# Kernel optimization log

Measured on AMD Instinct MI355X. Metric: run time of the kernel, lower is better.

## Reference

```python
import jax, jax.numpy as jnp
import numpy as np


def setup_inputs() -> dict:
    key = jax.random.key(0)
    kq, kk, kv, km, kb = jax.random.split(key, 5)
    B, H, S, D = 4, 16, 2048, 64
    Q = jax.random.normal(kq, (B, H, S, D), dtype=jnp.float32)
    K = jax.random.normal(kk, (B, H, S, D), dtype=jnp.float32)
    V = jax.random.normal(kv, (B, H, S, D), dtype=jnp.float32)
    # key-padding style mask, broadcasts over query dim; 0 -> masked
    mask = jax.random.randint(km, (B, 1, 1, S), 0, 2, dtype=jnp.int32)
    attn_bias = jax.random.normal(kb, (1, H, S, S), dtype=jnp.float32)
    return {"Q": Q, "K": K, "V": V, "mask": mask, "attn_bias": attn_bias}


def reference(Q, K, V, mask, attn_bias):
    d_k = Q.shape[-1]
    scale = 1.0 / jnp.sqrt(jnp.asarray(d_k, Q.dtype))
    # [B,H,Sq,Sk] scores
    scores = jnp.einsum("bhqd,bhkd->bhqk", Q, K) * scale
    scores = scores + attn_bias
    scores = jnp.where(mask == 0, jnp.asarray(-1e9, scores.dtype), scores)
    attn = jax.nn.softmax(scores, axis=-1)
    # dropout is identity in eval/reference mode
    output = jnp.einsum("bhqk,bhkd->bhqd", attn, V)
    return output, attn
```

## Files before the change

kernel.cpp:

```cpp
#include <hip/hip_runtime.h>

#define NB 4
#define NH 16
#define NS 2048
#define ND 64
#define PST 2052

typedef __attribute__((ext_vector_type(8))) short short8;
typedef __attribute__((ext_vector_type(4))) short short4v;
typedef __attribute__((ext_vector_type(4))) float floatx4;
typedef __attribute__((ext_vector_type(2))) float floatx2;

__device__ __forceinline__ unsigned short f2bf(float f) {
  unsigned u = __builtin_bit_cast(unsigned, f);
  u = (u + 0x7FFFu + ((u >> 16) & 1u)) >> 16;
  return (unsigned short)u;
}
__device__ __forceinline__ float bf2f(unsigned short s) {
  unsigned u = ((unsigned)s) << 16;
  return __builtin_bit_cast(float, u);
}

__global__ __launch_bounds__(256) void prep_k_kernel(const float* __restrict__ K,
                                                     unsigned short* __restrict__ kb) {
  size_t i = ((size_t)blockIdx.x * 256 + threadIdx.x) * 4;
  floatx4 v = *(const floatx4*)(K + i);
  unsigned long long o = 0;
  o |= (unsigned long long)f2bf(v[0]);
  o |= (unsigned long long)f2bf(v[1]) << 16;
  o |= (unsigned long long)f2bf(v[2]) << 32;
  o |= (unsigned long long)f2bf(v[3]) << 48;
  *(unsigned long long*)(kb + i) = o;
}

__global__ __launch_bounds__(256) void prep_vt_kernel(const float* __restrict__ V,
                                                      unsigned short* __restrict__ vt) {
  __shared__ float tile[64][65];
  int kc = blockIdx.x & 31;
  int bh = blockIdx.x >> 5;
  int k0 = kc * 64;
  const float* src = V + ((size_t)bh * NS + k0) * ND;
  int t = threadIdx.x;
  int r0 = t >> 4;
  int c = (t & 15) * 4;
  for (int rr = 0; rr < 4; ++rr) {
    int r = rr * 16 + r0;
    floatx4 v = *(const floatx4*)(src + (size_t)r * ND + c);
    tile[r][c + 0] = v[0]; tile[r][c + 1] = v[1];
    tile[r][c + 2] = v[2]; tile[r][c + 3] = v[3];
  }
  __syncthreads();
  unsigned short* dst = vt + (size_t)bh * ND * NS + k0;
  for (int i = 0; i < 16; ++i) {
    int lin = i * 256 + t;
    int d = lin >> 6, k = lin & 63;
    dst[(size_t)d * NS + k] = f2bf(tile[k][d]);
  }
}

__global__ __launch_bounds__(512, 4) void attn_kernel(
    const float* __restrict__ Q,
    const unsigned short* __restrict__ Kb,
    const unsigned short* __restrict__ VT,
    const int* __restrict__ mask,
    const float* __restrict__ bias,
    float* __restrict__ out,
    float* __restrict__ attn) {
  extern __shared__ char smem[];
  unsigned short* P = (unsigned short*)smem;
  float* sums = (float*)(smem + 16 * PST * 2);

  const int bid = blockIdx.x;
  const int b = bid & 3;
  const int qt = (bid >> 2) & 127;
  const int h = bid >> 9;
  const int q0 = qt * 16;

  const int tid = threadIdx.x;
  const int wave = tid >> 6;
  const int lane = tid & 63;
  const int lg = lane >> 4;
  const int lc = lane & 15;
  const int lg4 = lg * 4;
  const int lg8 = lg * 8;

  const size_t bh = (size_t)(b * NH + h);

  short8 aq[2];
  {
    const float* qrow = Q + (bh * NS + (size_t)(q0 + lc)) * ND + lg8;
#pragma unroll
    for (int t = 0; t < 2; ++t) {
      floatx4 f0 = *(const floatx4*)(qrow + t * 32);
      floatx4 f1 = *(const floatx4*)(qrow + t * 32 + 4);
      short8 a;
      a[0] = (short)f2bf(f0[0]); a[1] = (short)f2bf(f0[1]);
      a[2] = (short)f2bf(f0[2]); a[3] = (short)f2bf(f0[3]);
      a[4] = (short)f2bf(f1[0]); a[5] = (short)f2bf(f1[1]);
      a[6] = (short)f2bf(f1[2]); a[7] = (short)f2bf(f1[3]);
      aq[t] = a;
    }
  }

  const unsigned short* kp = Kb + bh * NS * ND + (size_t)lc * ND + lg8;
  const float* bprow = bias + ((size_t)h * NS + (size_t)(q0 + lg4)) * NS + lc;
  const int* mp = mask + b * NS + lc;
  const int kb0 = wave * 256;

  float psum[4] = {0.f, 0.f, 0.f, 0.f};

  short8 rka[4], rkb[4];
  floatx4 rbv[4];
  int rmv[4];
#pragma unroll
  for (int i = 0; i < 3; ++i) {
    const int k0 = kb0 + i * 16;
    rka[i] = *(const short8*)(kp + (size_t)k0 * ND);
    rkb[i] = *(const short8*)(kp + (size_t)k0 * ND + 32);
    rmv[i] = mp[k0];
    floatx4 bv;
#pragma unroll
    for (int r = 0; r < 4; ++r) bv[r] = bprow[(size_t)r * NS + k0];
    rbv[i] = bv;
  }
#pragma unroll
  for (int it = 0; it < 16; ++it) {
    const int s = it & 3;
    if (it < 13) {
      const int ps = (it + 3) & 3;
      const int k1 = kb0 + (it + 3) * 16;
      rka[ps] = *(const short8*)(kp + (size_t)k1 * ND);
      rkb[ps] = *(const short8*)(kp + (size_t)k1 * ND + 32);
      rmv[ps] = mp[k1];
      floatx4 bv;
#pragma unroll
      for (int r = 0; r < 4; ++r) bv[r] = bprow[(size_t)r * NS + k1];
      rbv[ps] = bv;
    }
    const int k0 = kb0 + it * 16;
    floatx4 c = {0.f, 0.f, 0.f, 0.f};
    c = __builtin_amdgcn_mfma_f32_16x16x32_bf16(aq[0], rka[s], c, 0, 0, 0);
    c = __builtin_amdgcn_mfma_f32_16x16x32_bf16(aq[1], rkb[s], c, 0, 0, 0);
    const int mv = rmv[s];
#pragma unroll
    for (int r = 0; r < 4; ++r) {
      float sc = c[r] * 0.125f + rbv[s][r];
      float p = mv ? __expf(sc) : 0.f;
      psum[r] += p;
      P[(lg4 + r) * PST + k0 + lc] = f2bf(p);
    }
  }

#pragma unroll
  for (int r = 0; r < 4; ++r) {
    float v = psum[r];
    v += __shfl_xor(v, 1);
    v += __shfl_xor(v, 2);
    v += __shfl_xor(v, 4);
    v += __shfl_xor(v, 8);
    if (lc == 0) sums[wave * 16 + lg4 + r] = v;
  }
  __syncthreads();

  const int wrow0 = wave * 2;
  float inv0, inv1;
  {
    float t0 = 0.f, t1 = 0.f;
#pragma unroll
    for (int w = 0; w < 8; ++w) {
      t0 += sums[w * 16 + wrow0];
      t1 += sums[w * 16 + wrow0 + 1];
    }
    inv0 = 1.f / t0;
    inv1 = 1.f / t1;
  }

  const size_t abase = (bh * NS + (size_t)q0) * NS;

#define WRITECHUNK(c)                                                        \
  {                                                                          \
    const int row_ = wrow0 + ((c) >> 3);                                     \
    const float inv_ = (((c) >> 3) == 0) ? inv0 : inv1;                      \
    const int col_ = ((c) & 7) * 256 + lane * 4;                             \
    short4v pv_ = *(const short4v*)(P + row_ * PST + col_);                  \
    floatx4 f_;                                                              \
    f_[0] = bf2f((unsigned short)pv_[0]) * inv_;                             \
    f_[1] = bf2f((unsigned short)pv_[1]) * inv_;                             \
    f_[2] = bf2f((unsigned short)pv_[2]) * inv_;                             \
    f_[3] = bf2f((unsigned short)pv_[3]) * inv_;                             \
    __builtin_nontemporal_store(f_, (floatx4*)(attn + abase +                \
                                               (size_t)row_ * NS + col_));   \
  }

  floatx4 o[4];
#pragma unroll
  for (int dt = 0; dt < 4; ++dt) o[dt] = (floatx4){0.f, 0.f, 0.f, 0.f};

  const unsigned short* vp = VT + bh * (size_t)ND * NS + (size_t)lc * NS + lg8;
  short8 vt0[4], vt1[4];
#pragma unroll
  for (int dt = 0; dt < 4; ++dt)
    vt0[dt] = *(const short8*)(vp + (size_t)(dt * 16) * NS + kb0);

#pragma unroll
  for (int ih = 0; ih < 4; ++ih) {
    const int itA = ih * 2, itB = ih * 2 + 1;
    const int k0A = kb0 + itA * 32, k0B = kb0 + itB * 32;
#pragma unroll
    for (int dt = 0; dt < 4; ++dt)
      vt1[dt] = *(const short8*)(vp + (size_t)(dt * 16) * NS + k0B);
    WRITECHUNK(ih * 4 + 0);
    WRITECHUNK(ih * 4 + 1);
    {
      const unsigned short* pr = P + lc * PST + k0A + lg8;
      short4v lo = *(const short4v*)pr;
      short4v hi = *(const short4v*)(pr + 4);
      short8 pa = __builtin_shufflevector(lo, hi, 0, 1, 2, 3, 4, 5, 6, 7);
#pragma unroll
      for (int dt = 0; dt < 4; ++dt)
        o[dt] = __builtin_amdgcn_mfma_f32_16x16x32_bf16(pa, vt0[dt], o[dt], 0, 0, 0);
    }
    if (ih < 3) {
      const int k0N = kb0 + (ih + 1) * 64;
#pragma unroll
      for (int dt = 0; dt < 4; ++dt)
        vt0[dt] = *(const short8*)(vp + (size_t)(dt * 16) * NS + k0N);
    }
    WRITECHUNK(ih * 4 + 2);
    WRITECHUNK(ih * 4 + 3);
    {
      const unsigned short* pr = P + lc * PST + k0B + lg8;
      short4v lo = *(const short4v*)pr;
      short4v hi = *(const short4v*)(pr + 4);
      short8 pa = __builtin_shufflevector(lo, hi, 0, 1, 2, 3, 4, 5, 6, 7);
#pragma unroll
      for (int dt = 0; dt < 4; ++dt)
        o[dt] = __builtin_amdgcn_mfma_f32_16x16x32_bf16(pa, vt1[dt], o[dt], 0, 0, 0);
    }
  }
#undef WRITECHUNK

  __syncthreads();

  float* Ored = (float*)smem;
#pragma unroll
  for (int dt = 0; dt < 4; ++dt)
#pragma unroll
    for (int r = 0; r < 4; ++r)
      Ored[((size_t)wave * 16 + lg4 + r) * 64 + dt * 16 + lc] = o[dt][r];
  __syncthreads();

  {
    const int q = tid >> 5;
    const int c2 = (tid & 31) * 2;
    floatx2 acc = {0.f, 0.f};
#pragma unroll
    for (int w = 0; w < 8; ++w) {
      const float* p = Ored + ((size_t)w * 16 + q) * 64 + c2;
      acc[0] += p[0];
      acc[1] += p[1];
    }
    float tot = 0.f;
#pragma unroll
    for (int w = 0; w < 8; ++w) tot += sums[w * 16 + q];
    const float inv = 1.f / tot;
    floatx2 res;
    res[0] = acc[0] * inv;
    res[1] = acc[1] * inv;
    __builtin_nontemporal_store(res, (floatx2*)(out + (bh * NS + (size_t)(q0 + q)) * ND + c2));
  }
}

extern "C" void kernel_launch(void* const* d_in, const int* in_sizes, int n_in,
                              void* d_out, int out_size, void* d_ws, size_t ws_size,
                              hipStream_t stream) {
  const float* Q = (const float*)d_in[0];
  const float* K = (const float*)d_in[1];
  const float* V = (const float*)d_in[2];
  const int* mask = (const int*)d_in[3];
  const float* bias = (const float*)d_in[4];

  float* out = (float*)d_out;
  float* attn = out + (size_t)NB * NH * NS * ND;

  unsigned short* kb = (unsigned short*)d_ws;
  unsigned short* vt = kb + (size_t)NB * NH * NS * ND;

  const int lds_bytes = 16 * PST * 2 + 8 * 16 * 4;
  (void)hipFuncSetAttribute((const void*)attn_kernel,
                            hipFuncAttributeMaxDynamicSharedMemorySize, lds_bytes);

  prep_k_kernel<<<(NB * NH * NS * ND) / (256 * 4), 256, 0, stream>>>(K, kb);
  prep_vt_kernel<<<NB * NH * (NS / 64), 256, 0, stream>>>(V, vt);
  attn_kernel<<<NB * NH * (NS / 16), 512, lds_bytes, stream>>>(Q, kb, vt, mask, bias, out, attn);
}
```

Baseline: 634.4 us.

## Transpose QK MFMA so bias and mask load as vectors, fold scale into Q

Swaps the MFMA operand order in the QK^T stage so each lane holds four consecutive keys for one query row. Bias and mask can then be read as 16-byte vectors, and the bias is used directly as the MFMA accumulator init. The 1/sqrt(d) scale is folded into Q before the bf16 conversion, and the row-sum reduction is simplified. The loops are manually unrolled into explicit register buffers with compiler memory fences to control load scheduling. Applying the scale before rounding to bf16 changes rounding slightly, and the fences may restrict compiler reordering.

Result: slower. 846.1 us (+33.4%).

```diff
diff --git a/kernel.cpp b/kernel.cpp
--- a/kernel.cpp
+++ b/kernel.cpp
@@ -10,6 +10,8 @@
 typedef __attribute__((ext_vector_type(4))) short short4v;
 typedef __attribute__((ext_vector_type(4))) float floatx4;
 typedef __attribute__((ext_vector_type(2))) float floatx2;
+typedef __attribute__((ext_vector_type(4))) int intx4;
+typedef __attribute__((ext_vector_type(2))) unsigned uintx2;
 
 __device__ __forceinline__ unsigned short f2bf(float f) {
   unsigned u = __builtin_bit_cast(unsigned, f);
@@ -86,80 +88,81 @@
 
   const size_t bh = (size_t)(b * NH + h);
 
-  short8 aq[2];
+  short8 aq0, aq1;
   {
     const float* qrow = Q + (bh * NS + (size_t)(q0 + lc)) * ND + lg8;
-#pragma unroll
-    for (int t = 0; t < 2; ++t) {
-      floatx4 f0 = *(const floatx4*)(qrow + t * 32);
-      floatx4 f1 = *(const floatx4*)(qrow + t * 32 + 4);
-      short8 a;
-      a[0] = (short)f2bf(f0[0]); a[1] = (short)f2bf(f0[1]);
-      a[2] = (short)f2bf(f0[2]); a[3] = (short)f2bf(f0[3]);
-      a[4] = (short)f2bf(f1[0]); a[5] = (short)f2bf(f1[1]);
-      a[6] = (short)f2bf(f1[2]); a[7] = (short)f2bf(f1[3]);
-      aq[t] = a;
+    floatx4 f0 = *(const floatx4*)(qrow);
+    floatx4 f1 = *(const floatx4*)(qrow + 4);
+    floatx4 f2 = *(const floatx4*)(qrow + 32);
+    floatx4 f3 = *(const floatx4*)(qrow + 36);
+#pragma unroll
+    for (int j = 0; j < 4; ++j) {
+      aq0[j] = (short)f2bf(f0[j] * 0.125f);
+      aq0[4 + j] = (short)f2bf(f1[j] * 0.125f);
+      aq1[j] = (short)f2bf(f2[j] * 0.125f);
+      aq1[4 + j] = (short)f2bf(f3[j] * 0.125f);
     }
   }
 
   const unsigned short* kp = Kb + bh * NS * ND + (size_t)lc * ND + lg8;
-  const float* bprow = bias + ((size_t)h * NS + (size_t)(q0 + lg4)) * NS + lc;
-  const int* mp = mask + b * NS + lc;
-  const int kb0 = wave * 256;
-
-  float psum[4] = {0.f, 0.f, 0.f, 0.f};
-
-  short8 rka[4], rkb[4];
-  floatx4 rbv[4];
-  int rmv[4];
-#pragma unroll
-  for (int i = 0; i < 3; ++i) {
-    const int k0 = kb0 + i * 16;
-    rka[i] = *(const short8*)(kp + (size_t)k0 * ND);
-    rkb[i] = *(const short8*)(kp + (size_t)k0 * ND + 32);
-    rmv[i] = mp[k0];
-    floatx4 bv;
-#pragma unroll
-    for (int r = 0; r < 4; ++r) bv[r] = bprow[(size_t)r * NS + k0];
-    rbv[i] = bv;
-  }
-#pragma unroll
-  for (int it = 0; it < 16; ++it) {
-    const int s = it & 3;
-    if (it < 13) {
-      const int ps = (it + 3) & 3;
-      const int k1 = kb0 + (it + 3) * 16;
-      rka[ps] = *(const short8*)(kp + (size_t)k1 * ND);
-      rkb[ps] = *(const short8*)(kp + (size_t)k1 * ND + 32);
-      rmv[ps] = mp[k1];
-      floatx4 bv;
-#pragma unroll
-      for (int r = 0; r < 4; ++r) bv[r] = bprow[(size_t)r * NS + k1];
-      rbv[ps] = bv;
-    }
-    const int k0 = kb0 + it * 16;
-    floatx4 c = {0.f, 0.f, 0.f, 0.f};
-    c = __builtin_amdgcn_mfma_f32_16x16x32_bf16(aq[0], rka[s], c, 0, 0, 0);
-    c = __builtin_amdgcn_mfma_f32_16x16x32_bf16(aq[1], rkb[s], c, 0, 0, 0);
-    const int mv = rmv[s];
-#pragma unroll
-    for (int r = 0; r < 4; ++r) {
-      float sc = c[r] * 0.125f + rbv[s][r];
-      float p = mv ? __expf(sc) : 0.f;
-      psum[r] += p;
-      P[(lg4 + r) * PST + k0 + lc] = f2bf(p);
-    }
-  }
-
-#pragma unroll
-  for (int r = 0; r < 4; ++r) {
-    float v = psum[r];
-    v += __shfl_xor(v, 1);
-    v += __shfl_xor(v, 2);
-    v += __shfl_xor(v, 4);
-    v += __shfl_xor(v, 8);
-    if (lc == 0) sums[wave * 16 + lg4 + r] = v;
-  }
+  const float* bp = bias + ((size_t)h * NS + (size_t)(q0 + lc)) * NS + lg4;
+  const int* mp = mask + b * NS + lg4;
+  const int ksb = wave * 256;
+  float psum = 0.f;
+
+  short8 kA0, kA1, kA2, kA3, kB0, kB1, kB2, kB3;
+  floatx4 bV0, bV1, bV2, bV3;
+  intx4 mV0, mV1, mV2, mV3;
+
+#define FENCE asm volatile("" ::: "memory")
+
+#define QK_LOAD(S, IT) {                                              \
+    const int k0_ = ksb + (IT) * 16;                                  \
+    kA##S = *(const short8*)(kp + (size_t)k0_ * ND);                  \
+    kB##S = *(const short8*)(kp + (size_t)k0_ * ND + 32);             \
+    bV##S = *(const floatx4*)(bp + k0_);                              \
+    mV##S = *(const intx4*)(mp + k0_);                                \
+  }
+
+#define QK_COMP(S, IT) {                                              \
+    const int k0_ = ksb + (IT) * 16;                                  \
+    floatx4 c;                                                        \
+    c[0] = bV##S[0]; c[1] = bV##S[1];                                 \
+    c[2] = bV##S[2]; c[3] = bV##S[3];                                 \
+    c = __builtin_amdgcn_mfma_f32_16x16x32_bf16(kA##S, aq0, c, 0, 0, 0); \
+    c = __builtin_amdgcn_mfma_f32_16x16x32_bf16(kB##S, aq1, c, 0, 0, 0); \
+    float p0 = mV##S[0] ? __expf(c[0]) : 0.f;                         \
+    float p1 = mV##S[1] ? __expf(c[1]) : 0.f;                         \
+    float p2 = mV##S[2] ? __expf(c[2]) : 0.f;                         \
+    float p3 = mV##S[3] ? __expf(c[3]) : 0.f;                         \
+    psum += (p0 + p1) + (p2 + p3);                                    \
+    uintx2 w_;                                                        \
+    w_[0] = (unsigned)f2bf(p0) | ((unsigned)f2bf(p1) << 16);          \
+    w_[1] = (unsigned)f2bf(p2) | ((unsigned)f2bf(p3) << 16);          \
+    *(uintx2*)((char*)P + (size_t)lc * (PST * 2) + (size_t)(k0_ + lg4) * 2) = w_; \
+  }
+
+  QK_LOAD(0, 0) QK_LOAD(1, 1) QK_LOAD(2, 2) FENCE;
+  QK_LOAD(3, 3)  FENCE; QK_COMP(0, 0)
+  QK_LOAD(0, 4)  FENCE; QK_COMP(1, 1)
+  QK_LOAD(1, 5)  FENCE; QK_COMP(2, 2)
+  QK_LOAD(2, 6)  FENCE; QK_COMP(3, 3)
+  QK_LOAD(3, 7)  FENCE; QK_COMP(0, 4)
+  QK_LOAD(0, 8)  FENCE; QK_COMP(1, 5)
+  QK_LOAD(1, 9)  FENCE; QK_COMP(2, 6)
+  QK_LOAD(2, 10) FENCE; QK_COMP(3, 7)
+  QK_LOAD(3, 11) FENCE; QK_COMP(0, 8)
+  QK_LOAD(0, 12) FENCE; QK_COMP(1, 9)
+  QK_LOAD(1, 13) FENCE; QK_COMP(2, 10)
+  QK_LOAD(2, 14) FENCE; QK_COMP(3, 11)
+  QK_LOAD(3, 15) FENCE; QK_COMP(0, 12)
+  QK_COMP(1, 13) QK_COMP(2, 14) QK_COMP(3, 15)
+#undef QK_LOAD
+#undef QK_COMP
+
+  psum += __shfl_xor(psum, 16);
+  psum += __shfl_xor(psum, 32);
+  if (lane < 16) sums[wave * 16 + lane] = psum;
   __syncthreads();
 
   const int wrow0 = wave * 2;
@@ -177,11 +180,10 @@
 
   const size_t abase = (bh * NS + (size_t)q0) * NS;
 
-#define WRITECHUNK(c)                                                        \
-  {                                                                          \
-    const int row_ = wrow0 + ((c) >> 3);                                     \
-    const float inv_ = (((c) >> 3) == 0) ? inv0 : inv1;                      \
-    const int col_ = ((c) & 7) * 256 + lane * 4;                             \
+#define WRITECHUNK(CI) {                                                     \
+    const int row_ = wrow0 + ((CI) >> 3);                                    \
+    const float inv_ = (((CI) >> 3) == 0) ? inv0 : inv1;                     \
+    const int col_ = ((CI) & 7) * 256 + lane * 4;                            \
     short4v pv_ = *(const short4v*)(P + row_ * PST + col_);                  \
     floatx4 f_;                                                              \
     f_[0] = bf2f((unsigned short)pv_[0]) * inv_;                             \
@@ -192,62 +194,54 @@
                                                (size_t)row_ * NS + col_));   \
   }
 
-  floatx4 o[4];
-#pragma unroll
-  for (int dt = 0; dt < 4; ++dt) o[dt] = (floatx4){0.f, 0.f, 0.f, 0.f};
-
+  floatx4 o0 = {0.f, 0.f, 0.f, 0.f}, o1 = {0.f, 0.f, 0.f, 0.f};
+  floatx4 o2 = {0.f, 0.f, 0.f, 0.f}, o3 = {0.f, 0.f, 0.f, 0.f};
   const unsigned short* vp = VT + bh * (size_t)ND * NS + (size_t)lc * NS + lg8;
-  short8 vt0[4], vt1[4];
-#pragma unroll
-  for (int dt = 0; dt < 4; ++dt)
-    vt0[dt] = *(const short8*)(vp + (size_t)(dt * 16) * NS + kb0);
-
-#pragma unroll
-  for (int ih = 0; ih < 4; ++ih) {
-    const int itA = ih * 2, itB = ih * 2 + 1;
-    const int k0A = kb0 + itA * 32, k0B = kb0 + itB * 32;
-#pragma unroll
-    for (int dt = 0; dt < 4; ++dt)
-      vt1[dt] = *(const short8*)(vp + (size_t)(dt * 16) * NS + k0B);
-    WRITECHUNK(ih * 4 + 0);
-    WRITECHUNK(ih * 4 + 1);
-    {
-      const unsigned short* pr = P + lc * PST + k0A + lg8;
-      short4v lo = *(const short4v*)pr;
-      short4v hi = *(const short4v*)(pr + 4);
-      short8 pa = __builtin_shufflevector(lo, hi, 0, 1, 2, 3, 4, 5, 6, 7);
-#pragma unroll
-      for (int dt = 0; dt < 4; ++dt)
-        o[dt] = __builtin_amdgcn_mfma_f32_16x16x32_bf16(pa, vt0[dt], o[dt], 0, 0, 0);
-    }
-    if (ih < 3) {
-      const int k0N = kb0 + (ih + 1) * 64;
-#pragma unroll
-      for (int dt = 0; dt < 4; ++dt)
-        vt0[dt] = *(const short8*)(vp + (size_t)(dt * 16) * NS + k0N);
-    }
-    WRITECHUNK(ih * 4 + 2);
-    WRITECHUNK(ih * 4 + 3);
-    {
-      const unsigned short* pr = P + lc * PST + k0B + lg8;
-      short4v lo = *(const short4v*)pr;
-      short4v hi = *(const short4v*)(pr + 4);
-      short8 pa = __builtin_shufflevector(lo, hi, 0, 1, 2, 3, 4, 5, 6, 7);
-#pragma unroll
-      for (int dt = 0; dt < 4; ++dt)
-        o[dt] = __builtin_amdgcn_mfma_f32_16x16x32_bf16(pa, vt1[dt], o[dt], 0, 0, 0);
-    }
-  }
+
+  short8 va0, va1, va2, va3, vb0, vb1, vb2, vb3;
+
+#define PV_LOAD(BUF, IT) {                                      \
+    const int k0_ = ksb + (IT) * 32;                            \
+    BUF##0 = *(const short8*)(vp + (size_t)(0 * 16) * NS + k0_); \
+    BUF##1 = *(const short8*)(vp + (size_t)(1 * 16) * NS + k0_); \
+    BUF##2 = *(const short8*)(vp + (size_t)(2 * 16) * NS + k0_); \
+    BUF##3 = *(const short8*)(vp + (size_t)(3 * 16) * NS + k0_); \
+  }
+
+#define PV_COMP(BUF, IT) {                                              \
+    const int k0_ = ksb + (IT) * 32;                                    \
+    const unsigned short* pr = P + (size_t)lc * PST + k0_ + lg8;        \
+    short4v lo = *(const short4v*)pr;                                   \
+    short4v hi = *(const short4v*)(pr + 4);                             \
+    short8 pa = __builtin_shufflevector(lo, hi, 0, 1, 2, 3, 4, 5, 6, 7); \
+    o0 = __builtin_amdgcn_mfma_f32_16x16x32_bf16(pa, BUF##0, o0, 0, 0, 0); \
+    o1 = __builtin_amdgcn_mfma_f32_16x16x32_bf16(pa, BUF##1, o1, 0, 0, 0); \
+    o2 = __builtin_amdgcn_mfma_f32_16x16x32_bf16(pa, BUF##2, o2, 0, 0, 0); \
+    o3 = __builtin_amdgcn_mfma_f32_16x16x32_bf16(pa, BUF##3, o3, 0, 0, 0); \
+  }
+
+  PV_LOAD(va, 0)
+  PV_LOAD(vb, 1) WRITECHUNK(0)  WRITECHUNK(1)  FENCE; PV_COMP(va, 0)
+  PV_LOAD(va, 2) WRITECHUNK(2)  WRITECHUNK(3)  FENCE; PV_COMP(vb, 1)
+  PV_LOAD(vb, 3) WRITECHUNK(4)  WRITECHUNK(5)  FENCE; PV_COMP(va, 2)
+  PV_LOAD(va, 4) WRITECHUNK(6)  WRITECHUNK(7)  FENCE; PV_COMP(vb, 3)
+  PV_LOAD(vb, 5) WRITECHUNK(8)  WRITECHUNK(9)  FENCE; PV_COMP(va, 4)
+  PV_LOAD(va, 6) WRITECHUNK(10) WRITECHUNK(11) FENCE; PV_COMP(vb, 5)
+  PV_LOAD(vb, 7) WRITECHUNK(12) WRITECHUNK(13) FENCE; PV_COMP(va, 6)
+  WRITECHUNK(14) WRITECHUNK(15) FENCE; PV_COMP(vb, 7)
+#undef PV_LOAD
+#undef PV_COMP
 #undef WRITECHUNK
 
   __syncthreads();
 
   float* Ored = (float*)smem;
-#pragma unroll
-  for (int dt = 0; dt < 4; ++dt)
-#pragma unroll
-    for (int r = 0; r < 4; ++r)
-      Ored[((size_t)wave * 16 + lg4 + r) * 64 + dt * 16 + lc] = o[dt][r];
+#define OWRITE(OV, DT) {                                                   \
+    _Pragma("unroll") for (int r = 0; r < 4; ++r)                          \
+      Ored[((size_t)wave * 16 + lg4 + r) * 64 + (DT) * 16 + lc] = OV[r];   \
+  }
+  OWRITE(o0, 0) OWRITE(o1, 1) OWRITE(o2, 2) OWRITE(o3, 3)
+#undef OWRITE
   __syncthreads();
 
   {
```
